# Kernel optimization log

Hardware: AMD Instinct MI355X
Metric: run time of the kernel (lower is better)

## Reference

```python
import jax, jax.numpy as jnp
import numpy as np

TOP_K = 2


def setup_inputs() -> dict:
    key = jax.random.key(0)
    ks = jax.random.split(key, 6)
    B, S, D, H, E = 2, 2048, 1024, 4096, 8
    s_in = 1.0 / np.sqrt(D)
    s_hid = 1.0 / np.sqrt(H)
    return {
        "x": jax.random.normal(ks[0], (B, S, D), jnp.float32),
        "Wg": jax.random.normal(ks[1], (E, D), jnp.float32) * s_in,
        "W1": jax.random.normal(ks[2], (E, D, H), jnp.float32) * s_in,
        "b1": jax.random.normal(ks[3], (E, H), jnp.float32) * 0.01,
        "W2": jax.random.normal(ks[4], (E, H, D), jnp.float32) * s_hid,
        "b2": jax.random.normal(ks[5], (E, D), jnp.float32) * 0.01,
    }


def reference(x, Wg, W1, b1, W2, b2):
    B, S, D = x.shape
    E = Wg.shape[0]
    T = B * S
    xf = x.reshape(T, D)

    # ---- router ----
    logits = xf @ Wg.T                              # (T, E)
    probs = jax.nn.softmax(logits, axis=-1)
    top_v, top_i = jax.lax.top_k(probs, TOP_K)      # (T, k)
    top_v = top_v / top_v.sum(axis=-1, keepdims=True)

    # aux load-balancing loss
    expert_mask = jax.nn.one_hot(top_i, E, dtype=probs.dtype).sum(axis=1)  # (T, E)
    f = expert_mask.mean(axis=0)
    p = probs.mean(axis=0)
    aux_loss = E * (f * p).sum()

    # ---- combine weights: scatter normalized top-k probs into (T, E) ----
    w = jnp.zeros((T, E), probs.dtype).at[jnp.arange(T)[:, None], top_i].add(top_v)

    # ---- all-expert FFN (grouped GEMM form), weighted combine ----
    h = jax.nn.silu(jnp.einsum('td,edh->teh', xf, W1) + b1[None])   # (T, E, H)
    y = jnp.einsum('teh,ehd->ted', h, W2) + b2[None]                # (T, E, D)
    out = jnp.einsum('ted,te->td', y, w)                            # (T, D)
    return out.reshape(B, S, D), aux_loss
```

## Files before the change

### kernel.cpp

```cpp
#include <hip/hip_runtime.h>
#include <cstdint>
#include <cstddef>

#define T_TOK 4096
#define DIM   1024
#define HID   4096
#define NE    8
#define PAD   128
#define PADMAX 9216
#define KSPLIT2 4

typedef _Float16 half_t;
typedef __attribute__((ext_vector_type(8))) _Float16 half8;
typedef __attribute__((ext_vector_type(4))) float floatx4;

__device__ __forceinline__ float silu_f(float v) {
  return v / (1.0f + expf(-v));
}

__device__ __forceinline__ half8 cvt44(float4 a, float4 b) {
  half8 o;
  o[0] = (half_t)a.x; o[1] = (half_t)a.y; o[2] = (half_t)a.z; o[3] = (half_t)a.w;
  o[4] = (half_t)b.x; o[5] = (half_t)b.y; o[6] = (half_t)b.z; o[7] = (half_t)b.w;
  return o;
}

__device__ __forceinline__ void gload16(const void* g, void* l) {
  __builtin_amdgcn_global_load_lds(
      (const __attribute__((address_space(1))) unsigned int*)g,
      (__attribute__((address_space(3))) unsigned int*)l, 16, 0, 0);
}

__device__ __forceinline__ int xcd_swz(int lin, int Nw) {
  int q = Nw >> 3;
  return (lin & 7) * q + (lin >> 3);
}

__global__ void k_reset(float* prob_sum, unsigned* cnt, unsigned* cursor,
                        int* pair_tok, float* pair_wt) {
  int i = blockIdx.x * 256 + threadIdx.x;
  if (i < PADMAX) { pair_tok[i] = 0; pair_wt[i] = 0.0f; }
  if (i < NE) { prob_sum[i] = 0.0f; cnt[i] = 0u; cursor[i] = 0u; }
}

__global__ __launch_bounds__(256) void k_cvt_x(const float* __restrict__ x,
                                               half_t* __restrict__ xh) {
  size_t i = (size_t)blockIdx.x * 256 + threadIdx.x;
  const float4* s = (const float4*)(x + i * 8);
  float4 a = s[0], b = s[1];
  *(half8*)(xh + i * 8) = cvt44(a, b);
}

__global__ __launch_bounds__(256) void k_tr_w1(const float* __restrict__ W1,
                                               half_t* __restrict__ W1t,
                                               int j0, int Hc) {
  __shared__ half_t T[64][72];
  int e = blockIdx.z, h0 = blockIdx.x * 64, d0 = blockIdx.y * 64;
  int tid = threadIdx.x;
  {
    int r = tid >> 2, c16 = (tid & 3) * 16;
    const float* s = W1 + ((size_t)e * DIM + d0 + r) * HID + j0 + h0 + c16;
    float4 a = ((const float4*)s)[0], b = ((const float4*)s)[1];
    float4 c = ((const float4*)s)[2], d = ((const float4*)s)[3];
    *(half8*)&T[r][c16] = cvt44(a, b);
    *(half8*)&T[r][c16 + 8] = cvt44(c, d);
  }
  __syncthreads();
  {
    int n = tid >> 2, d16 = (tid & 3) * 16;
    half8 u, v;
#pragma unroll
    for (int j = 0; j < 8; ++j) { u[j] = T[d16 + j][n]; v[j] = T[d16 + 8 + j][n]; }
    half_t* dst = W1t + ((size_t)e * Hc + h0 + n) * DIM + d0 + d16;
    *(half8*)dst = u;
    *(half8*)(dst + 8) = v;
  }
}

__global__ __launch_bounds__(256) void k_tr_w2(const float* __restrict__ W2,
                                               half_t* __restrict__ W2t,
                                               int j0, int Hc) {
  __shared__ half_t T[64][72];
  int e = blockIdx.z, d0 = blockIdx.x * 64, h0 = blockIdx.y * 64;
  int tid = threadIdx.x;
  {
    int r = tid >> 2, c16 = (tid & 3) * 16;
    const float* s = W2 + ((size_t)e * HID + j0 + h0 + r) * DIM + d0 + c16;
    float4 a = ((const float4*)s)[0], b = ((const float4*)s)[1];
    float4 c = ((const float4*)s)[2], d = ((const float4*)s)[3];
    *(half8*)&T[r][c16] = cvt44(a, b);
    *(half8*)&T[r][c16 + 8] = cvt44(c, d);
  }
  __syncthreads();
  {
    int n = tid >> 2, h16 = (tid & 3) * 16;
    half8 u, v;
#pragma unroll
    for (int j = 0; j < 8; ++j) { u[j] = T[h16 + j][n]; v[j] = T[h16 + 8 + j][n]; }
    half_t* dst = W2t + ((size_t)e * DIM + d0 + n) * Hc + h0 + h16;
    *(half8*)dst = u;
    *(half8*)(dst + 8) = v;
  }
}

__global__ __launch_bounds__(256) void k_router(
    const float* __restrict__ x, const float* __restrict__ Wg,
    int* __restrict__ top_i, float* __restrict__ top_w,
    float* __restrict__ prob_sum, unsigned* __restrict__ cnt) {
  __shared__ float sWg[NE * DIM];
  __shared__ float sProb[NE];
  __shared__ unsigned sCnt[NE];
  int tid = threadIdx.x;
  if (tid < NE) { sProb[tid] = 0.0f; sCnt[tid] = 0u; }
  for (int i = tid; i < NE * DIM; i += 256) sWg[i] = Wg[i];
  __syncthreads();

  int wave = tid >> 6, lane = tid & 63;
  for (int it = 0; it < 4; ++it) {
    int t = blockIdx.x * 16 + wave * 4 + it;
    const float* xp = x + (size_t)t * DIM;
    float acc[NE];
#pragma unroll
    for (int e = 0; e < NE; ++e) acc[e] = 0.0f;
    for (int i = 0; i < DIM / 64; ++i) {
      int d = i * 64 + lane;
      float xd = xp[d];
#pragma unroll
      for (int e = 0; e < NE; ++e) acc[e] = fmaf(xd, sWg[e * DIM + d], acc[e]);
    }
#pragma unroll
    for (int off = 32; off > 0; off >>= 1)
#pragma unroll
      for (int e = 0; e < NE; ++e) acc[e] += __shfl_xor(acc[e], off, 64);

    if (lane == 0) {
      float m = acc[0];
#pragma unroll
      for (int e = 1; e < NE; ++e) m = fmaxf(m, acc[e]);
      float pr[NE]; float s = 0.0f;
#pragma unroll
      for (int e = 0; e < NE; ++e) { pr[e] = expf(acc[e] - m); s += pr[e]; }
      float inv = 1.0f / s;
#pragma unroll
      for (int e = 0; e < NE; ++e) pr[e] *= inv;
      int i0 = 0; float v0 = pr[0];
#pragma unroll
      for (int e = 1; e < NE; ++e) if (pr[e] > v0) { v0 = pr[e]; i0 = e; }
      int i1 = -1; float v1 = -1.0f;
#pragma unroll
      for (int e = 0; e < NE; ++e) if (e != i0 && pr[e] > v1) { v1 = pr[e]; i1 = e; }
      float wn = 1.0f / (v0 + v1);
      top_i[t * 2 + 0] = i0; top_i[t * 2 + 1] = i1;
      top_w[t * 2 + 0] = v0 * wn; top_w[t * 2 + 1] = v1 * wn;
#pragma unroll
      for (int e = 0; e < NE; ++e) atomicAdd(&sProb[e], pr[e]);
      atomicAdd(&sCnt[i0], 1u);
      atomicAdd(&sCnt[i1], 1u);
    }
  }
  __syncthreads();
  if (tid < NE) {
    atomicAdd(&prob_sum[tid], sProb[tid]);
    atomicAdd(&cnt[tid], sCnt[tid]);
  }
}

__global__ void k_scan(const unsigned* __restrict__ cnt,
                       const float* __restrict__ prob_sum,
                       int* __restrict__ pad_off, int* __restrict__ ptotal,
                       float* __restrict__ aux_out) {
  if (threadIdx.x == 0 && blockIdx.x == 0) {
    int off = 0; float aux = 0.0f;
    for (int e = 0; e < NE; ++e) {
      pad_off[e] = off;
      off += (int)((cnt[e] + (PAD - 1u)) & ~(unsigned)(PAD - 1));
      aux += ((float)cnt[e] / (float)T_TOK) * (prob_sum[e] / (float)T_TOK);
    }
    pad_off[NE] = off;
    *ptotal = off;
    *aux_out = (float)NE * aux;
  }
}

__global__ void k_scatter(const int* __restrict__ top_i, const float* __restrict__ top_w,
                          const int* __restrict__ pad_off, unsigned* __restrict__ cursor,
                          int* __restrict__ pair_tok, float* __restrict__ pair_wt) {
  int t = blockIdx.x * 256 + threadIdx.x;
  if (t >= T_TOK) return;
#pragma unroll
  for (int k = 0; k < 2; ++k) {
    int e = top_i[t * 2 + k];
    unsigned pos = atomicAdd(&cursor[e], 1u);
    int idx = pad_off[e] + (int)pos;
    pair_tok[idx] = t;
    pair_wt[idx]  = top_w[t * 2 + k];
  }
}

__global__ void k_init_out(const int* __restrict__ top_i, const float* __restrict__ top_w,
                           const float* __restrict__ b2, float* __restrict__ out) {
  int idx = blockIdx.x * 256 + threadIdx.x;
  int t = idx >> 10, d = idx & (DIM - 1);
  int e0 = top_i[t * 2 + 0], e1 = top_i[t * 2 + 1];
  out[idx] = top_w[t * 2 + 0] * b2[e0 * DIM + d] + top_w[t * 2 + 1] * b2[e1 * DIM + d];
}

__global__ __launch_bounds__(256) void k_gemm1_a(
    const half_t* __restrict__ xh, const half_t* __restrict__ W1t,
    const float* __restrict__ b1, const int* __restrict__ pair_tok,
    const int* __restrict__ pad_off, const int* __restrict__ ptotal,
    half_t* __restrict__ hout, int j0, int Hc) {
  __shared__ half_t lds[16384];
  int wid = xcd_swz(blockIdx.x, gridDim.x);
  int col = wid / (PADMAX / 128);
  int row = wid % (PADMAX / 128);
  int P = *ptotal;
  int p0 = row * 128;
  if (p0 >= P) return;
  int e = 0;
#pragma unroll
  for (int q = 1; q < NE; ++q) if (p0 >= pad_off[q]) e = q;

  int tid = threadIdx.x, w = tid >> 6, l = tid & 63;
  int lr = l & 15, lq = l >> 4;
  int wr = w >> 1, wc = w & 1;
  int jt = col * 128;

  int tok0 = pair_tok[p0 + (2 * w) * 16 + lr];
  int tok1 = pair_tok[p0 + (2 * w + 1) * 16 + lr];
  const half_t* gA0 = xh + (size_t)tok0 * DIM + lq * 8;
  const half_t* gA1 = xh + (size_t)tok1 * DIM + lq * 8;
  const half_t* gB0 = W1t + ((size_t)e * Hc + jt + (2 * w) * 16 + lr) * DIM + lq * 8;
  const half_t* gB1 = W1t + ((size_t)e * Hc + jt + (2 * w + 1) * 16 + lr) * DIM + lq * 8;

  half_t* ldsA = lds;
  half_t* ldsB = lds + 8192;
  half_t* dA = ldsA + (4 * w) * 512;
  half_t* dB = ldsB + (4 * w) * 512;

  floatx4 acc[4][4];
#pragma unroll
  for (int i = 0; i < 4; ++i)
#pragma unroll
    for (int j = 0; j < 4; ++j) acc[i][j] = (floatx4){0.f, 0.f, 0.f, 0.f};

  for (int kt = 0; kt < DIM; kt += 64) {
    __syncthreads();
    gload16(gA0 + kt,      dA + 0 * 512);
    gload16(gA0 + kt + 32, dA + 1 * 512);
    gload16(gA1 + kt,      dA + 2 * 512);
    gload16(gA1 + kt + 32, dA + 3 * 512);
    gload16(gB0 + kt,      dB + 0 * 512);
    gload16(gB0 + kt + 32, dB + 1 * 512);
    gload16(gB1 + kt,      dB + 2 * 512);
    gload16(gB1 + kt + 32, dB + 3 * 512);
    __syncthreads();
#pragma unroll
    for (int ks = 0; ks < 2; ++ks) {
      half8 a[4], b[4];
#pragma unroll
      for (int i = 0; i < 4; ++i)
        a[i] = *(const half8*)(ldsA + ((4 * wr + i) * 2 + ks) * 512 + l * 8);
#pragma unroll
      for (int j = 0; j < 4; ++j)
        b[j] = *(const half8*)(ldsB + ((4 * wc + j) * 2 + ks) * 512 + l * 8);
#pragma unroll
      for (int i = 0; i < 4; ++i)
#pragma unroll
        for (int j = 0; j < 4; ++j)
          acc[i][j] = __builtin_amdgcn_mfma_f32_16x16x32_f16(a[i], b[j], acc[i][j], 0, 0, 0);
    }
  }
  __syncthreads();

#pragma unroll
  for (int j = 0; j < 4; ++j) {
    int coll = (4 * wc + j) * 16 + lr;
    float bias = b1[(size_t)e * HID + j0 + jt + coll];
#pragma unroll
    for (int i = 0; i < 4; ++i)
#pragma unroll
      for (int r = 0; r < 4; ++r) {
        int row2 = (4 * wr + i) * 16 + lq * 4 + r;
        lds[row2 * 128 + coll] = (half_t)silu_f(acc[i][j][r] + bias);
      }
  }
  __syncthreads();
#pragma unroll
  for (int ps = 0; ps < 4; ++ps) {
    int r = ps * 32 + (tid >> 3), c = (tid & 7) * 16;
    half8 v0 = *(const half8*)(lds + r * 128 + c);
    half8 v1 = *(const half8*)(lds + r * 128 + c + 8);
    half_t* dst = hout + (size_t)(p0 + r) * Hc + jt + c;
    *(half8*)dst = v0;
    *(half8*)(dst + 8) = v1;
  }
}

__global__ __launch_bounds__(256) void k_gemm2_a(
    const half_t* __restrict__ hbuf, const half_t* __restrict__ W2t,
    const int* __restrict__ pair_tok, const float* __restrict__ pair_wt,
    const int* __restrict__ pad_off, const int* __restrict__ ptotal,
    float* __restrict__ out, int Hc) {
  __shared__ half_t lds[16384];
  int wid = xcd_swz(blockIdx.x, gridDim.x);
  int c  = wid & 7;
  int rz = wid >> 3;
  int row = rz % (PADMAX / 128);
  int zk  = rz / (PADMAX / 128);
  int P = *ptotal;
  int p0 = row * 128;
  if (p0 >= P) return;
  int e = 0;
#pragma unroll
  for (int q = 1; q < NE; ++q) if (p0 >= pad_off[q]) e = q;

  int tid = threadIdx.x, w = tid >> 6, l = tid & 63;
  int lr = l & 15, lq = l >> 4;
  int wr = w >> 1, wc = w & 1;
  int jt = c * 128;

  int ks_total = Hc >> 6;
  int kt_beg = ((zk * ks_total) / KSPLIT2) * 64;
  int kt_end = (((zk + 1) * ks_total) / KSPLIT2) * 64;

  const half_t* gA0 = hbuf + (size_t)(p0 + (2 * w) * 16 + lr) * Hc + lq * 8;
  const half_t* gA1 = hbuf + (size_t)(p0 + (2 * w + 1) * 16 + lr) * Hc + lq * 8;
  const half_t* gB0 = W2t + ((size_t)e * DIM + jt + (2 * w) * 16 + lr) * Hc + lq * 8;
  const half_t* gB1 = W2t + ((size_t)e * DIM + jt + (2 * w + 1) * 16 + lr) * Hc + lq * 8;

  half_t* ldsA = lds;
  half_t* ldsB = lds + 8192;
  half_t* dA = ldsA + (4 * w) * 512;
  half_t* dB = ldsB + (4 * w) * 512;

  floatx4 acc[4][4];
#pragma unroll
  for (int i = 0; i < 4; ++i)
#pragma unroll
    for (int j = 0; j < 4; ++j) acc[i][j] = (floatx4){0.f, 0.f, 0.f, 0.f};

  for (int kt = kt_beg; kt < kt_end; kt += 64) {
    __syncthreads();
    gload16(gA0 + kt,      dA + 0 * 512);
    gload16(gA0 + kt + 32, dA + 1 * 512);
    gload16(gA1 + kt,      dA + 2 * 512);
    gload16(gA1 + kt + 32, dA + 3 * 512);
    gload16(gB0 + kt,      dB + 0 * 512);
    gload16(gB0 + kt + 32, dB + 1 * 512);
    gload16(gB1 + kt,      dB + 2 * 512);
    gload16(gB1 + kt + 32, dB + 3 * 512);
    __syncthreads();
#pragma unroll
    for (int ks = 0; ks < 2; ++ks) {
      half8 a[4], b[4];
#pragma unroll
      for (int i = 0; i < 4; ++i)
        a[i] = *(const half8*)(ldsA + ((4 * wr + i) * 2 + ks) * 512 + l * 8);
#pragma unroll
      for (int j = 0; j < 4; ++j)
        b[j] = *(const half8*)(ldsB + ((4 * wc + j) * 2 + ks) * 512 + l * 8);
#pragma unroll
      for (int i = 0; i < 4; ++i)
#pragma unroll
        for (int j = 0; j < 4; ++j)
          acc[i][j] = __builtin_amdgcn_mfma_f32_16x16x32_f16(a[i], b[j], acc[i][j], 0, 0, 0);
    }
  }

#pragma unroll
  for (int i = 0; i < 4; ++i)
#pragma unroll
    for (int r = 0; r < 4; ++r) {
      int row2 = (4 * wr + i) * 16 + lq * 4 + r;
      float wt = pair_wt[p0 + row2];
      if (wt != 0.0f) {
        int tok = pair_tok[p0 + row2];
        float* op = out + (size_t)tok * DIM + jt;
#pragma unroll
        for (int j = 0; j < 4; ++j) {
          int coll = (4 * wc + j) * 16 + lr;
          unsafeAtomicAdd(op + coll, wt * acc[i][j][r]);
        }
      }
    }
}

__global__ __launch_bounds__(256) void k_gemm1_b(
    const half_t* __restrict__ xh, const float* __restrict__ W1,
    const float* __restrict__ b1, const int* __restrict__ pair_tok,
    const int* __restrict__ pad_off, const int* __restrict__ ptotal,
    half_t* __restrict__ hout, int j0, int Hc) {
  __shared__ half_t lds[16384];
  int P = *ptotal;
  int p0 = blockIdx.y * 128;
  if (p0 >= P) return;
  int e = 0;
#pragma unroll
  for (int q = 1; q < NE; ++q) if (p0 >= pad_off[q]) e = q;

  int tid = threadIdx.x, w = tid >> 6, l = tid & 63;
  int lr = l & 15, lq = l >> 4;
  int wr = w >> 1, wc = w & 1;
  int jt = blockIdx.x * 128;

  int tok0 = pair_tok[p0 + (2 * w) * 16 + lr];
  int tok1 = pair_tok[p0 + (2 * w + 1) * 16 + lr];
  const half_t* gA0 = xh + (size_t)tok0 * DIM + lq * 8;
  const half_t* gA1 = xh + (size_t)tok1 * DIM + lq * 8;
  const float* gBb = W1 + (size_t)e * DIM * HID + j0 + jt;
  const float* gB0 = gBb + (2 * w) * 16 + lr;
  const float* gB1 = gBb + (2 * w + 1) * 16 + lr;

  half_t* ldsA = lds;
  half_t* ldsB = lds + 8192;

  floatx4 acc[4][4];
#pragma unroll
  for (int i = 0; i < 4; ++i)
#pragma unroll
    for (int j = 0; j < 4; ++j) acc[i][j] = (floatx4){0.f, 0.f, 0.f, 0.f};

  for (int kt = 0; kt < DIM; kt += 64) {
    half8 va0 = *(const half8*)(gA0 + kt);
    half8 va1 = *(const half8*)(gA0 + kt + 32);
    half8 va2 = *(const half8*)(gA1 + kt);
    half8 va3 = *(const half8*)(gA1 + kt + 32);
    half8 vb[4];
#pragma unroll
    for (int fg = 0; fg < 4; ++fg) {
      const float* gb = (fg >> 1) ? gB1 : gB0;
      int kbase = kt + (fg & 1) * 32 + lq * 8;
#pragma unroll
      for (int j = 0; j < 8; ++j)
        vb[fg][j] = (half_t)gb[(size_t)(kbase + j) * HID];
    }
    __syncthreads();
    *(half8*)(ldsA + (4 * w + 0) * 512 + l * 8) = va0;
    *(half8*)(ldsA + (4 * w + 1) * 512 + l * 8) = va1;
    *(half8*)(ldsA + (4 * w + 2) * 512 + l * 8) = va2;
    *(half8*)(ldsA + (4 * w + 3) * 512 + l * 8) = va3;
    *(half8*)(ldsB + (4 * w + 0) * 512 + l * 8) = vb[0];
    *(half8*)(ldsB + (4 * w + 1) * 512 + l * 8) = vb[1];
    *(half8*)(ldsB + (4 * w + 2) * 512 + l * 8) = vb[2];
    *(half8*)(ldsB + (4 * w + 3) * 512 + l * 8) = vb[3];
    __syncthreads();
#pragma unroll
    for (int ks = 0; ks < 2; ++ks) {
      half8 a[4], b[4];
#pragma unroll
      for (int i = 0; i < 4; ++i)
        a[i] = *(const half8*)(ldsA + ((4 * wr + i) * 2 + ks) * 512 + l * 8);
#pragma unroll
      for (int j = 0; j < 4; ++j)
        b[j] = *(const half8*)(ldsB + ((4 * wc + j) * 2 + ks) * 512 + l * 8);
#pragma unroll
      for (int i = 0; i < 4; ++i)
#pragma unroll
        for (int j = 0; j < 4; ++j)
          acc[i][j] = __builtin_amdgcn_mfma_f32_16x16x32_f16(a[i], b[j], acc[i][j], 0, 0, 0);
    }
  }
  __syncthreads();

#pragma unroll
  for (int j = 0; j < 4; ++j) {
    int coll = (4 * wc + j) * 16 + lr;
    float bias = b1[(size_t)e * HID + j0 + jt + coll];
#pragma unroll
    for (int i = 0; i < 4; ++i)
#pragma unroll
      for (int r = 0; r < 4; ++r) {
        int row = (4 * wr + i) * 16 + lq * 4 + r;
        lds[row * 128 + coll] = (half_t)silu_f(acc[i][j][r] + bias);
      }
  }
  __syncthreads();
#pragma unroll
  for (int ps = 0; ps < 4; ++ps) {
    int r = ps * 32 + (tid >> 3), c = (tid & 7) * 16;
    half8 v0 = *(const half8*)(lds + r * 128 + c);
    half8 v1 = *(const half8*)(lds + r * 128 + c + 8);
    half_t* dst = hout + (size_t)(p0 + r) * Hc + jt + c;
    *(half8*)dst = v0;
    *(half8*)(dst + 8) = v1;
  }
}

__global__ __launch_bounds__(256) void k_gemm2_b(
    const half_t* __restrict__ hbuf, const float* __restrict__ W2,
    const int* __restrict__ pair_tok, const float* __restrict__ pair_wt,
    const int* __restrict__ pad_off, const int* __restrict__ ptotal,
    float* __restrict__ out, int j0, int Hc) {
  __shared__ half_t lds[16384];
  int P = *ptotal;
  int p0 = blockIdx.y * 128;
  if (p0 >= P) return;
  int e = 0;
#pragma unroll
  for (int q = 1; q < NE; ++q) if (p0 >= pad_off[q]) e = q;

  int tid = threadIdx.x, w = tid >> 6, l = tid & 63;
  int lr = l & 15, lq = l >> 4;
  int wr = w >> 1, wc = w & 1;
  int jt = blockIdx.x * 128;

  const half_t* gA0 = hbuf + (size_t)(p0 + (2 * w) * 16 + lr) * Hc + lq * 8;
  const half_t* gA1 = hbuf + (size_t)(p0 + (2 * w + 1) * 16 + lr) * Hc + lq * 8;
  const float* gBb = W2 + (size_t)e * HID * DIM + jt;
  const float* gB0 = gBb + (2 * w) * 16 + lr;
  const float* gB1 = gBb + (2 * w + 1) * 16 + lr;

  half_t* ldsA = lds;
  half_t* ldsB = lds + 8192;

  floatx4 acc[4][4];
#pragma unroll
  for (int i = 0; i < 4; ++i)
#pragma unroll
    for (int j = 0; j < 4; ++j) acc[i][j] = (floatx4){0.f, 0.f, 0.f, 0.f};

  for (int kt = 0; kt < Hc; kt += 64) {
    half8 va0 = *(const half8*)(gA0 + kt);
    half8 va1 = *(const half8*)(gA0 + kt + 32);
    half8 va2 = *(const half8*)(gA1 + kt);
    half8 va3 = *(const half8*)(gA1 + kt + 32);
    half8 vb[4];
#pragma unroll
    for (int fg = 0; fg < 4; ++fg) {
      const float* gb = (fg >> 1) ? gB1 : gB0;
      int kbase = j0 + kt + (fg & 1) * 32 + lq * 8;
#pragma unroll
      for (int j = 0; j < 8; ++j)
        vb[fg][j] = (half_t)gb[(size_t)(kbase + j) * DIM];
    }
    __syncthreads();
    *(half8*)(ldsA + (4 * w + 0) * 512 + l * 8) = va0;
    *(half8*)(ldsA + (4 * w + 1) * 512 + l * 8) = va1;
    *(half8*)(ldsA + (4 * w + 2) * 512 + l * 8) = va2;
    *(half8*)(ldsA + (4 * w + 3) * 512 + l * 8) = va3;
    *(half8*)(ldsB + (4 * w + 0) * 512 + l * 8) = vb[0];
    *(half8*)(ldsB + (4 * w + 1) * 512 + l * 8) = vb[1];
    *(half8*)(ldsB + (4 * w + 2) * 512 + l * 8) = vb[2];
    *(half8*)(ldsB + (4 * w + 3) * 512 + l * 8) = vb[3];
    __syncthreads();
#pragma unroll
    for (int ks = 0; ks < 2; ++ks) {
      half8 a[4], b[4];
#pragma unroll
      for (int i = 0; i < 4; ++i)
        a[i] = *(const half8*)(ldsA + ((4 * wr + i) * 2 + ks) * 512 + l * 8);
#pragma unroll
      for (int j = 0; j < 4; ++j)
        b[j] = *(const half8*)(ldsB + ((4 * wc + j) * 2 + ks) * 512 + l * 8);
#pragma unroll
      for (int i = 0; i < 4; ++i)
#pragma unroll
        for (int j = 0; j < 4; ++j)
          acc[i][j] = __builtin_amdgcn_mfma_f32_16x16x32_f16(a[i], b[j], acc[i][j], 0, 0, 0);
    }
  }

#pragma unroll
  for (int i = 0; i < 4; ++i)
#pragma unroll
    for (int r = 0; r < 4; ++r) {
      int row = (4 * wr + i) * 16 + lq * 4 + r;
      float wt = pair_wt[p0 + row];
      if (wt != 0.0f) {
        int tok = pair_tok[p0 + row];
        float* op = out + (size_t)tok * DIM + jt;
#pragma unroll
        for (int j = 0; j < 4; ++j) {
          int coll = (4 * wc + j) * 16 + lr;
          unsafeAtomicAdd(op + coll, wt * acc[i][j][r]);
        }
      }
    }
}

extern "C" void kernel_launch(void* const* d_in, const int* in_sizes, int n_in,
                              void* d_out, int out_size, void* d_ws, size_t ws_size,
                              hipStream_t stream) {
  const float* x  = (const float*)d_in[0];
  const float* Wg = (const float*)d_in[1];
  const float* W1 = (const float*)d_in[2];
  const float* b1 = (const float*)d_in[3];
  const float* W2 = (const float*)d_in[4];
  const float* b2 = (const float*)d_in[5];
  float* out = (float*)d_out;

  char* p = (char*)d_ws;
  auto alloc = [&](size_t bytes) -> char* {
    char* r = p; p += (bytes + 255) & ~(size_t)255; return r;
  };
  int*      top_i    = (int*)     alloc((size_t)T_TOK * 2 * sizeof(int));
  float*    top_w    = (float*)   alloc((size_t)T_TOK * 2 * sizeof(float));
  float*    prob_sum = (float*)   alloc(NE * sizeof(float));
  unsigned* cnt      = (unsigned*)alloc(NE * sizeof(unsigned));
  int*      pad_off  = (int*)     alloc((NE + 1) * sizeof(int));
  int*      ptotal   = (int*)     alloc(sizeof(int));
  unsigned* cursor   = (unsigned*)alloc(NE * sizeof(unsigned));
  int*      pair_tok = (int*)     alloc(PADMAX * sizeof(int));
  float*    pair_wt  = (float*)   alloc(PADMAX * sizeof(float));
  half_t*   xh       = (half_t*)  alloc((size_t)T_TOK * DIM * sizeof(half_t));

  size_t used  = (size_t)(p - (char*)d_ws);
  size_t avail = ws_size > used ? ws_size - used : 0;

  size_t per_col_a = (size_t)2 * NE * DIM * sizeof(half_t) + (size_t)PADMAX * sizeof(half_t);
  int HcA = (int)((avail / per_col_a) & ~(size_t)127);
  if (HcA > HID) HcA = HID;
  bool modeA = (HcA >= 128);

  k_reset<<<dim3((PADMAX + 255) / 256), 256, 0, stream>>>(prob_sum, cnt, cursor, pair_tok, pair_wt);
  k_cvt_x<<<dim3((size_t)T_TOK * DIM / 8 / 256), 256, 0, stream>>>(x, xh);
  k_router<<<dim3(T_TOK / 16), 256, 0, stream>>>(x, Wg, top_i, top_w, prob_sum, cnt);
  k_scan<<<1, 64, 0, stream>>>(cnt, prob_sum, pad_off, ptotal, out + (size_t)T_TOK * DIM);
  k_scatter<<<dim3(T_TOK / 256), 256, 0, stream>>>(top_i, top_w, pad_off, cursor, pair_tok, pair_wt);
  k_init_out<<<dim3((size_t)T_TOK * DIM / 256), 256, 0, stream>>>(top_i, top_w, b2, out);

  if (modeA) {
    int Hc = HcA;
    half_t* W1t  = (half_t*)alloc((size_t)NE * Hc * DIM * sizeof(half_t));
    half_t* W2t  = (half_t*)alloc((size_t)NE * DIM * Hc * sizeof(half_t));
    half_t* hbuf = (half_t*)alloc((size_t)PADMAX * Hc * sizeof(half_t));
    for (int jb = 0; jb < HID; jb += Hc) {
      int hc = (HID - jb) < Hc ? (HID - jb) : Hc;
      k_tr_w1<<<dim3(hc / 64, DIM / 64, NE), 256, 0, stream>>>(W1, W1t, jb, hc);
      k_gemm1_a<<<dim3((hc / 128) * (PADMAX / 128)), 256, 0, stream>>>(
          xh, W1t, b1, pair_tok, pad_off, ptotal, hbuf, jb, hc);
      k_tr_w2<<<dim3(DIM / 64, hc / 64, NE), 256, 0, stream>>>(W2, W2t, jb, hc);
      k_gemm2_a<<<dim3((DIM / 128) * (PADMAX / 128) * KSPLIT2), 256, 0, stream>>>(
          hbuf, W2t, pair_tok, pair_wt, pad_off, ptotal, out, hc);
    }
  } else {
    int Hc = (int)((avail / ((size_t)PADMAX * sizeof(half_t))) & ~(size_t)127);
    if (Hc > HID) Hc = HID;
    if (Hc < 128) Hc = 128;
    half_t* hbuf = (half_t*)alloc((size_t)PADMAX * Hc * sizeof(half_t));
    for (int jb = 0; jb < HID; jb += Hc) {
      int hc = (HID - jb) < Hc ? (HID - jb) : Hc;
      k_gemm1_b<<<dim3(hc / 128, PADMAX / 128), 256, 0, stream>>>(
          xh, W1, b1, pair_tok, pad_off, ptotal, hbuf, jb, hc);
      k_gemm2_b<<<dim3(DIM / 128, PADMAX / 128), 256, 0, stream>>>(
          hbuf, W2, pair_tok, pair_wt, pad_off, ptotal, out, jb, hc);
    }
  }
}
```

Measured before the change: 748.3 us.

## Pre-tile weights and hidden buffer into MFMA fragment order for contiguous loads

The weight transpose kernels now write W1 and W2 as 64x128 tiles stored directly in the per-lane MFMA fragment order. gemm1 writes its hidden output in the same tiled layout. Each wave's global-to-LDS loads for the weight and hidden operands then become fully contiguous 8 KB blocks instead of strided row reads. The gemm2 K-split is also reduced from 4 to 2, which halves the atomic partial-sum traffic into the output but also halves the number of blocks.

```diff
diff --git a/kernel.cpp b/kernel.cpp
--- a/kernel.cpp
+++ b/kernel.cpp
@@ -8,7 +8,7 @@
 #define NE    8
 #define PAD   128
 #define PADMAX 9216
-#define KSPLIT2 4
+#define KSPLIT2 2
 
 typedef _Float16 half_t;
 typedef __attribute__((ext_vector_type(8))) _Float16 half8;
@@ -34,6 +34,24 @@
 __device__ __forceinline__ int xcd_swz(int lin, int Nw) {
   int q = Nw >> 3;
   return (lin & 7) * q + (lin >> 3);
+}
+
+
+__device__ __forceinline__ void write_tiled(const half_t* sT, half_t* dstTile, int tid) {
+#pragma unroll
+  for (int t2 = 0; t2 < 4; ++t2) {
+    int o = (t2 * 256 + tid) * 8;
+    int m = o >> 9, p2 = o & 511;
+    int lane2 = p2 >> 3;
+    int rg = ((m >> 2) << 1) | ((m >> 1) & 1);
+    int khalf = m & 1;
+    int fr = rg * 16 + (lane2 & 15);
+    int fk = khalf * 32 + (lane2 >> 4) * 8;
+    half8 v;
+#pragma unroll
+    for (int j = 0; j < 8; ++j) v[j] = sT[(fk + j) * 136 + fr];
+    *(half8*)(dstTile + o) = v;
+  }
 }
 
 __global__ void k_reset(float* prob_sum, unsigned* cnt, unsigned* cursor,
@@ -52,55 +70,45 @@
 }
 
 __global__ __launch_bounds__(256) void k_tr_w1(const float* __restrict__ W1,
-                                               half_t* __restrict__ W1t,
+                                               half_t* __restrict__ W1c,
                                                int j0, int Hc) {
-  __shared__ half_t T[64][72];
-  int e = blockIdx.z, h0 = blockIdx.x * 64, d0 = blockIdx.y * 64;
+  __shared__ half_t sT[64 * 136];
+  int e = blockIdx.z, J = blockIdx.x, Kd = blockIdx.y;
   int tid = threadIdx.x;
   {
-    int r = tid >> 2, c16 = (tid & 3) * 16;
-    const float* s = W1 + ((size_t)e * DIM + d0 + r) * HID + j0 + h0 + c16;
-    float4 a = ((const float4*)s)[0], b = ((const float4*)s)[1];
-    float4 c = ((const float4*)s)[2], d = ((const float4*)s)[3];
-    *(half8*)&T[r][c16] = cvt44(a, b);
-    *(half8*)&T[r][c16 + 8] = cvt44(c, d);
-  }
-  __syncthreads();
-  {
-    int n = tid >> 2, d16 = (tid & 3) * 16;
-    half8 u, v;
-#pragma unroll
-    for (int j = 0; j < 8; ++j) { u[j] = T[d16 + j][n]; v[j] = T[d16 + 8 + j][n]; }
-    half_t* dst = W1t + ((size_t)e * Hc + h0 + n) * DIM + d0 + d16;
-    *(half8*)dst = u;
-    *(half8*)(dst + 8) = v;
-  }
+    int rr = tid >> 2, q = tid & 3;
+    const float* s = W1 + ((size_t)e * DIM + Kd * 64 + rr) * HID + j0 + J * 128 + q * 32;
+    float4 f[8];
+#pragma unroll
+    for (int i = 0; i < 8; ++i) f[i] = ((const float4*)s)[i];
+    half_t* d = sT + rr * 136 + q * 32;
+#pragma unroll
+    for (int i = 0; i < 4; ++i) *(half8*)(d + i * 8) = cvt44(f[2 * i], f[2 * i + 1]);
+  }
+  __syncthreads();
+  half_t* dstTile = W1c + (((size_t)e * (Hc >> 7) + J) * (DIM / 64) + Kd) * 8192;
+  write_tiled(sT, dstTile, tid);
 }
 
 __global__ __launch_bounds__(256) void k_tr_w2(const float* __restrict__ W2,
-                                               half_t* __restrict__ W2t,
+                                               half_t* __restrict__ W2c,
                                                int j0, int Hc) {
-  __shared__ half_t T[64][72];
-  int e = blockIdx.z, d0 = blockIdx.x * 64, h0 = blockIdx.y * 64;
+  __shared__ half_t sT[64 * 136];
+  int e = blockIdx.z, J = blockIdx.x, K2 = blockIdx.y;
   int tid = threadIdx.x;
   {
-    int r = tid >> 2, c16 = (tid & 3) * 16;
-    const float* s = W2 + ((size_t)e * HID + j0 + h0 + r) * DIM + d0 + c16;
-    float4 a = ((const float4*)s)[0], b = ((const float4*)s)[1];
-    float4 c = ((const float4*)s)[2], d = ((const float4*)s)[3];
-    *(half8*)&T[r][c16] = cvt44(a, b);
-    *(half8*)&T[r][c16 + 8] = cvt44(c, d);
-  }
-  __syncthreads();
-  {
-    int n = tid >> 2, h16 = (tid & 3) * 16;
-    half8 u, v;
-#pragma unroll
-    for (int j = 0; j < 8; ++j) { u[j] = T[h16 + j][n]; v[j] = T[h16 + 8 + j][n]; }
-    half_t* dst = W2t + ((size_t)e * DIM + d0 + n) * Hc + h0 + h16;
-    *(half8*)dst = u;
-    *(half8*)(dst + 8) = v;
-  }
+    int hh = tid >> 2, q = tid & 3;
+    const float* s = W2 + ((size_t)e * HID + j0 + K2 * 64 + hh) * DIM + J * 128 + q * 32;
+    float4 f[8];
+#pragma unroll
+    for (int i = 0; i < 8; ++i) f[i] = ((const float4*)s)[i];
+    half_t* d = sT + hh * 136 + q * 32;
+#pragma unroll
+    for (int i = 0; i < 4; ++i) *(half8*)(d + i * 8) = cvt44(f[2 * i], f[2 * i + 1]);
+  }
+  __syncthreads();
+  half_t* dstTile = W2c + (((size_t)e * (DIM / 128) + J) * (Hc >> 6) + K2) * 8192;
+  write_tiled(sT, dstTile, tid);
 }
 
 __global__ __launch_bounds__(256) void k_router(
@@ -206,10 +214,10 @@
 }
 
 __global__ __launch_bounds__(256) void k_gemm1_a(
-    const half_t* __restrict__ xh, const half_t* __restrict__ W1t,
+    const half_t* __restrict__ xh, const half_t* __restrict__ W1c,
     const float* __restrict__ b1, const int* __restrict__ pair_tok,
     const int* __restrict__ pad_off, const int* __restrict__ ptotal,
-    half_t* __restrict__ hout, int j0, int Hc) {
+    half_t* __restrict__ hbuf, int j0, int Hc) {
   __shared__ half_t lds[16384];
   int wid = xcd_swz(blockIdx.x, gridDim.x);
   int col = wid / (PADMAX / 128);
@@ -224,19 +232,19 @@
   int tid = threadIdx.x, w = tid >> 6, l = tid & 63;
   int lr = l & 15, lq = l >> 4;
   int wr = w >> 1, wc = w & 1;
+  int w4 = 4 * w;
   int jt = col * 128;
 
   int tok0 = pair_tok[p0 + (2 * w) * 16 + lr];
   int tok1 = pair_tok[p0 + (2 * w + 1) * 16 + lr];
   const half_t* gA0 = xh + (size_t)tok0 * DIM + lq * 8;
   const half_t* gA1 = xh + (size_t)tok1 * DIM + lq * 8;
-  const half_t* gB0 = W1t + ((size_t)e * Hc + jt + (2 * w) * 16 + lr) * DIM + lq * 8;
-  const half_t* gB1 = W1t + ((size_t)e * Hc + jt + (2 * w + 1) * 16 + lr) * DIM + lq * 8;
+  const half_t* gBt = W1c + (((size_t)e * (Hc >> 7) + (jt >> 7)) * (DIM / 64)) * 8192 + l * 8;
 
   half_t* ldsA = lds;
   half_t* ldsB = lds + 8192;
-  half_t* dA = ldsA + (4 * w) * 512;
-  half_t* dB = ldsB + (4 * w) * 512;
+  half_t* dA = ldsA + w4 * 512;
+  half_t* dB = ldsB + w4 * 512;
 
   floatx4 acc[4][4];
 #pragma unroll
@@ -244,16 +252,16 @@
 #pragma unroll
     for (int j = 0; j < 4; ++j) acc[i][j] = (floatx4){0.f, 0.f, 0.f, 0.f};
 
-  for (int kt = 0; kt < DIM; kt += 64) {
+  for (int s = 0; s < DIM / 64; ++s) {
+    int kt = s * 64;
     __syncthreads();
     gload16(gA0 + kt,      dA + 0 * 512);
     gload16(gA0 + kt + 32, dA + 1 * 512);
     gload16(gA1 + kt,      dA + 2 * 512);
     gload16(gA1 + kt + 32, dA + 3 * 512);
-    gload16(gB0 + kt,      dB + 0 * 512);
-    gload16(gB0 + kt + 32, dB + 1 * 512);
-    gload16(gB1 + kt,      dB + 2 * 512);
-    gload16(gB1 + kt + 32, dB + 3 * 512);
+    const half_t* gBs = gBt + (size_t)s * 8192;
+#pragma unroll
+    for (int i = 0; i < 4; ++i) gload16(gBs + (w4 + i) * 512, dB + i * 512);
     __syncthreads();
 #pragma unroll
     for (int ks = 0; ks < 2; ++ks) {
@@ -286,19 +294,24 @@
       }
   }
   __syncthreads();
-#pragma unroll
-  for (int ps = 0; ps < 4; ++ps) {
-    int r = ps * 32 + (tid >> 3), c = (tid & 7) * 16;
-    half8 v0 = *(const half8*)(lds + r * 128 + c);
-    half8 v1 = *(const half8*)(lds + r * 128 + c + 8);
-    half_t* dst = hout + (size_t)(p0 + r) * Hc + jt + c;
-    *(half8*)dst = v0;
-    *(half8*)(dst + 8) = v1;
+  {
+    size_t tb = ((size_t)(p0 >> 7) * (Hc >> 6) + (jt >> 6)) * 8192;
+#pragma unroll
+    for (int t2 = 0; t2 < 8; ++t2) {
+      int o = (t2 * 256 + tid) * 8;
+      int kk = o >> 13, rem = o & 8191;
+      int m = rem >> 9, p2 = rem & 511;
+      int lane2 = p2 >> 3;
+      int rg = ((m >> 2) << 1) | ((m >> 1) & 1);
+      int rr = rg * 16 + (lane2 & 15);
+      int colb = kk * 64 + (m & 1) * 32 + (lane2 >> 4) * 8;
+      *(half8*)(hbuf + tb + o) = *(const half8*)(lds + rr * 128 + colb);
+    }
   }
 }
 
 __global__ __launch_bounds__(256) void k_gemm2_a(
-    const half_t* __restrict__ hbuf, const half_t* __restrict__ W2t,
+    const half_t* __restrict__ hbuf, const half_t* __restrict__ W2c,
     const int* __restrict__ pair_tok, const float* __restrict__ pair_wt,
     const int* __restrict__ pad_off, const int* __restrict__ ptotal,
     float* __restrict__ out, int Hc) {
@@ -318,21 +331,20 @@
   int tid = threadIdx.x, w = tid >> 6, l = tid & 63;
   int lr = l & 15, lq = l >> 4;
   int wr = w >> 1, wc = w & 1;
+  int w4 = 4 * w;
   int jt = c * 128;
 
-  int ks_total = Hc >> 6;
-  int kt_beg = ((zk * ks_total) / KSPLIT2) * 64;
-  int kt_end = (((zk + 1) * ks_total) / KSPLIT2) * 64;
-
-  const half_t* gA0 = hbuf + (size_t)(p0 + (2 * w) * 16 + lr) * Hc + lq * 8;
-  const half_t* gA1 = hbuf + (size_t)(p0 + (2 * w + 1) * 16 + lr) * Hc + lq * 8;
-  const half_t* gB0 = W2t + ((size_t)e * DIM + jt + (2 * w) * 16 + lr) * Hc + lq * 8;
-  const half_t* gB1 = W2t + ((size_t)e * DIM + jt + (2 * w + 1) * 16 + lr) * Hc + lq * 8;
+  int nkt = Hc >> 6;
+  int t_beg = (zk * nkt) / KSPLIT2;
+  int t_end = ((zk + 1) * nkt) / KSPLIT2;
+
+  const half_t* gA = hbuf + ((size_t)row * nkt) * 8192 + l * 8;
+  const half_t* gB = W2c + (((size_t)e * (DIM / 128) + c) * nkt) * 8192 + l * 8;
 
   half_t* ldsA = lds;
   half_t* ldsB = lds + 8192;
-  half_t* dA = ldsA + (4 * w) * 512;
-  half_t* dB = ldsB + (4 * w) * 512;
+  half_t* dA = ldsA + w4 * 512;
+  half_t* dB = ldsB + w4 * 512;
 
   floatx4 acc[4][4];
 #pragma unroll
@@ -340,16 +352,14 @@
 #pragma unroll
     for (int j = 0; j < 4; ++j) acc[i][j] = (floatx4){0.f, 0.f, 0.f, 0.f};
 
-  for (int kt = kt_beg; kt < kt_end; kt += 64) {
-    __syncthreads();
-    gload16(gA0 + kt,      dA + 0 * 512);
-    gload16(gA0 + kt + 32, dA + 1 * 512);
-    gload16(gA1 + kt,      dA + 2 * 512);
-    gload16(gA1 + kt + 32, dA + 3 * 512);
-    gload16(gB0 + kt,      dB + 0 * 512);
-    gload16(gB0 + kt + 32, dB + 1 * 512);
-    gload16(gB1 + kt,      dB + 2 * 512);
-    gload16(gB1 + kt + 32, dB + 3 * 512);
+  for (int s = t_beg; s < t_end; ++s) {
+    const half_t* gAs = gA + (size_t)s * 8192;
+    const half_t* gBs = gB + (size_t)s * 8192;
+    __syncthreads();
+#pragma unroll
+    for (int i = 0; i < 4; ++i) gload16(gAs + (w4 + i) * 512, dA + i * 512);
+#pragma unroll
+    for (int i = 0; i < 4; ++i) gload16(gBs + (w4 + i) * 512, dB + i * 512);
     __syncthreads();
 #pragma unroll
     for (int ks = 0; ks < 2; ++ks) {
@@ -622,17 +632,17 @@
 
   if (modeA) {
     int Hc = HcA;
-    half_t* W1t  = (half_t*)alloc((size_t)NE * Hc * DIM * sizeof(half_t));
-    half_t* W2t  = (half_t*)alloc((size_t)NE * DIM * Hc * sizeof(half_t));
+    half_t* W1c  = (half_t*)alloc((size_t)NE * Hc * DIM * sizeof(half_t));
+    half_t* W2c  = (half_t*)alloc((size_t)NE * DIM * Hc * sizeof(half_t));
     half_t* hbuf = (half_t*)alloc((size_t)PADMAX * Hc * sizeof(half_t));
     for (int jb = 0; jb < HID; jb += Hc) {
       int hc = (HID - jb) < Hc ? (HID - jb) : Hc;
-      k_tr_w1<<<dim3(hc / 64, DIM / 64, NE), 256, 0, stream>>>(W1, W1t, jb, hc);
+      k_tr_w1<<<dim3(hc / 128, DIM / 64, NE), 256, 0, stream>>>(W1, W1c, jb, hc);
       k_gemm1_a<<<dim3((hc / 128) * (PADMAX / 128)), 256, 0, stream>>>(
-          xh, W1t, b1, pair_tok, pad_off, ptotal, hbuf, jb, hc);
-      k_tr_w2<<<dim3(DIM / 64, hc / 64, NE), 256, 0, stream>>>(W2, W2t, jb, hc);
+          xh, W1c, b1, pair_tok, pad_off, ptotal, hbuf, jb, hc);
+      k_tr_w2<<<dim3(DIM / 128, hc / 64, NE), 256, 0, stream>>>(W2, W2c, jb, hc);
       k_gemm2_a<<<dim3((DIM / 128) * (PADMAX / 128) * KSPLIT2), 256, 0, stream>>>(
-          hbuf, W2t, pair_tok, pair_wt, pad_off, ptotal, out, hc);
+          hbuf, W2c, pair_tok, pair_wt, pad_off, ptotal, out, hc);
     }
   } else {
     int Hc = (int)((avail / ((size_t)PADMAX * sizeof(half_t))) & ~(size_t)127);
```

Result: faster. 626.3 us (-16.3%).
